# Kernel tuning notes

Measured on AMD Instinct MI355X. Metric: run time of the kernel, lower is better.

Reference implementation:

```python
import jax, jax.numpy as jnp
import numpy as np

B, N, T, NUM_API = 4, 160, 512, 20000  # queries, list length, tag vocab size, number of APIs
TAG_DENSITY = 0.05


def _compute_lambda(y_score, tag_set, M):
    # y_score: [N]; tag_set: [N,T] multi-hot rows api_tag_embedding[y_pred]; M: [T] multi-hot target.
    # Faithful to mode == 'cover' branch of LambdaRankLoss.compute_lambda.
    n = tag_set.shape[0]
    f32 = tag_set.dtype
    idx = jnp.arange(n)
    log_values = jnp.log2(jnp.arange(2, n + 2, dtype=f32))             # [N]
    P = jax.lax.cummax(tag_set, axis=0)                                # set_union_list = cummax(tag_set) [N,T]
    Mc = (jnp.count_nonzero(M) + 1).astype(f32)                        # M_nonzero_count
    # count_nonzero(clamp(M - set_union_list[k], min=0)) == #(M_t > P[k,t])
    cU = jnp.sum(M[None, :] > P, axis=1).astype(f32)                   # [N]

    # pre[i] = rowwise-max of tag_set[:i-1]. Torch quirk: i==0 -> tag_set[:-1] (all but last row); i==1 -> empty.
    pre = jnp.where(idx[:, None] == 0, P[n - 2][None, :],
                    jnp.where(idx[:, None] == 1, jnp.zeros((), f32),
                              P[jnp.clip(idx - 2, 0, n - 1)]))         # [N,T] (0 is max-identity: entries >= 0)

    # R[a,b] = max(tag_set[a..b]) along rows; 0 when b < a (rows before a masked to 0, then cummax)
    masked = jnp.where(idx[None, :, None] >= idx[:, None, None], tag_set[None, :, :], jnp.zeros((), f32))
    R = jax.lax.cummax(masked, axis=1)                                 # [N,N,T]

    # mid[k,i] = max(tag_set[i+1:k]) = R[i+1, k-1] when k >= i+2, else empty -> 0
    i_ix = idx[None, :]
    k_ix = idx[:, None]
    mid = jnp.where((k_ix >= i_ix + 2)[:, :, None],
                    R[jnp.clip(i_ix + 1, 0, n - 1), jnp.clip(k_ix - 1, 0, n - 1)],
                    jnp.zeros((), f32))                                # [K,I,T]

    # A[k,i] = max(cat(tag_set[:i-1], tag_set[i+1:k]));  Q[k,i,j] = max(A[k,i], tag_set[j])
    A = jnp.maximum(pre[None, :, :], mid)                              # [K,I,T]
    # count_nonzero(clamp(M - Q[k,i,j], 0)) = sum_t [M_t > A[k,i,t]] * [M_t > tag_set[j,t]]
    aM = (M[None, None, :] > A).astype(f32)                            # [K,I,T]
    bM = (M[None, :] > tag_set).astype(f32)                            # [J,T]
    cQ = jnp.einsum('kit,jt->kij', aM, bM)                             # [K,I,J] Q_nonzero counts

    W = (cU[:, None, None] - cQ) / (Mc * log_values[:, None, None])    # [K,I,J]
    # Z1[i,j] = sum_{k=i}^{j-1} W[k,i,j]  (strictly upper-triangular in (i,j))
    maskZ = (idx[None, :, None] <= idx[:, None, None]) & (idx[:, None, None] < idx[None, None, :])
    Z1 = jnp.sum(jnp.where(maskZ, W, jnp.zeros((), f32)), axis=0)      # [I,J]

    # lambda1[i,j] = 1 / (1 + exp(s_i - s_j))
    lam = 1.0 / (1.0 + jnp.exp(y_score[:, None] - y_score[None, :]))
    return jnp.sum(lam * Z1) / jnp.asarray(n + 1, f32)


def setup_inputs() -> dict:
    key = jax.random.key(0)
    k1, k2, k3, k4 = jax.random.split(key, 4)
    y_scores = jax.random.normal(k1, (B, N), jnp.float32)
    y_preds = jax.random.randint(k2, (B, N), 0, NUM_API)
    M = (jax.random.uniform(k3, (B, T)) < TAG_DENSITY).astype(jnp.float32)
    api_tag_embedding = (jax.random.uniform(k4, (NUM_API, T)) < TAG_DENSITY).astype(jnp.float32)
    return {"y_scores": y_scores, "M": M, "api_tag_embedding": api_tag_embedding, "y_preds": y_preds}


def reference(y_scores, M, api_tag_embedding, y_preds):
    def per_query(s, m, pred):
        return _compute_lambda(s, api_tag_embedding[pred], m)
    vals = jax.vmap(per_query)(y_scores, M, y_preds)  # [B]
    return jnp.mean(vals)  # loss / len(y_scores)
```

## Files before the change

### kernel.cpp

```cpp
#include <hip/hip_runtime.h>
#include <stdint.h>

typedef unsigned long long u64;

constexpr int B_ = 4;
constexpr int N_ = 160;
constexpr int T_ = 512;
constexpr int W_ = T_ / 64;

__global__ __launch_bounds__(64) void pack_tags(const float* __restrict__ emb,
                                                const int* __restrict__ preds,
                                                u64* __restrict__ tags,
                                                int* __restrict__ counter) {
    int row  = blockIdx.x;
    int lane = threadIdx.x;
    if (row == 0 && lane == 0) *counter = 0;
    const float* src = emb + (long long)preds[row] * T_;
#pragma unroll
    for (int w = 0; w < W_; ++w) {
        float v = src[w * 64 + lane];
        u64 m = __ballot(v != 0.0f);
        if (lane == 0) tags[(long long)row * W_ + w] = m;
    }
}

__global__ __launch_bounds__(256) void pack_scan(const float* __restrict__ Mf,
                                                 const u64* __restrict__ tags,
                                                 u64* __restrict__ Mp,
                                                 u64* __restrict__ P,
                                                 float* __restrict__ cU,
                                                 float* __restrict__ Mc) {
    __shared__ u64 S0[N_ * W_];
    __shared__ u64 S1[N_ * W_];
    __shared__ u64 Msh[W_];

    const int b    = blockIdx.x;
    const int tid  = threadIdx.x;
    const int lane = tid & 63;
    const int wv   = tid >> 6;

    for (int w = wv; w < W_; w += 4) {
        float v = Mf[(long long)b * T_ + w * 64 + lane];
        u64 m = __ballot(v != 0.0f);
        if (lane == 0) { Msh[w] = m; Mp[b * W_ + w] = m; }
    }
    for (int x = tid; x < N_ * W_; x += 256)
        S0[x] = tags[(long long)b * N_ * W_ + x];
    __syncthreads();

    u64* src = S0;
    u64* dst = S1;
    for (int d = 1; d < N_; d <<= 1) {
        for (int x = tid; x < N_ * W_; x += 256) {
            int r = x >> 3;
            u64 v = src[x];
            if (r >= d) v |= src[x - d * W_];
            dst[x] = v;
        }
        __syncthreads();
        u64* t = src; src = dst; dst = t;
    }

    for (int x = tid; x < N_ * W_; x += 256)
        P[(long long)b * N_ * W_ + x] = src[x];

    if (tid < N_) {
        int c = 0;
#pragma unroll
        for (int w = 0; w < W_; ++w)
            c += __popcll(Msh[w] & ~src[tid * W_ + w]);
        cU[b * N_ + tid] = (float)c;
    }
    if (tid == 0) {
        int c = 0;
#pragma unroll
        for (int w = 0; w < W_; ++w) c += __popcll(Msh[w]);
        Mc[b] = (float)(c + 1);
    }
}

__global__ __launch_bounds__(192) void lambda_main(const u64* __restrict__ tags,
                                                   const u64* __restrict__ Mp,
                                                   const u64* __restrict__ P,
                                                   const float* __restrict__ cU,
                                                   const float* __restrict__ Mc,
                                                   const float* __restrict__ scores,
                                                   double* __restrict__ partials,
                                                   int* __restrict__ counter,
                                                   float* __restrict__ out) {
    __shared__ u64 tagsL[N_ * W_];
    __shared__ u64 S0[N_ * W_];
    __shared__ u64 S1[N_ * W_];
    __shared__ u64 Msh[W_];
    __shared__ float scoresL[N_];
    __shared__ float redF[3];
    __shared__ int isLast;
    __shared__ double redD[3];

    const int k   = blockIdx.x;
    const int b   = blockIdx.y;
    const int tid = threadIdx.x;

    if (tid < W_) Msh[tid] = Mp[b * W_ + tid];
    for (int x = tid; x < N_; x += 192) scoresL[x] = scores[b * N_ + x];
    for (int x = tid; x < N_ * W_; x += 192)
        tagsL[x] = tags[(long long)b * N_ * W_ + x];
    __syncthreads();

    const int ne = k * W_;
    u64* src = S0;
    u64* dst = S1;
    for (int x = tid; x < ne; x += 192) src[x] = tagsL[x];
    __syncthreads();
    for (int d = 1; d < k; d <<= 1) {
        for (int x = tid; x < ne; x += 192) {
            int r = x >> 3;
            u64 v = src[x];
            if (r + d < k) v |= src[x + d * W_];
            dst[x] = v;
        }
        __syncthreads();
        u64* t = src; src = dst; dst = t;
    }

    u64* awL = dst;
    for (int x = tid; x < (k + 1) * W_; x += 192) {
        int i = x >> 3, w = x & 7;
        u64 pre;
        if (i == 1) pre = 0ull;
        else {
            int sr = (i == 0) ? (N_ - 2) : (i - 2);
            pre = P[((long long)b * N_ + sr) * W_ + w];
        }
        u64 sv = (i + 1 < k) ? src[(i + 1) * W_ + w] : 0ull;
        awL[x] = Msh[w] & ~pre & ~sv;
    }
    __syncthreads();

    const int m = N_ - 1 - k;
    float val = 0.0f;
    if (tid < m) {
        const int j = k + 1 + tid;
        u64 Bw[W_];
#pragma unroll
        for (int w = 0; w < W_; ++w) Bw[w] = Msh[w] & ~tagsL[j * W_ + w];
        const float sj  = scoresL[j];
        const float cUk = cU[b * N_ + k];
        float accLam = 0.0f, accC = 0.0f;
#pragma unroll 4
        for (int i = 0; i <= k; ++i) {
            int cc = 0;
#pragma unroll
            for (int w = 0; w < W_; ++w)
                cc += __popcll(awL[i * W_ + w] & Bw[w]);
            float lam = 1.0f / (1.0f + __expf(scoresL[i] - sj));
            accLam += lam;
            accC   += lam * (float)cc;
        }
        val = cUk * accLam - accC;
    }
    for (int off = 32; off >= 1; off >>= 1) val += __shfl_down(val, off, 64);
    if ((tid & 63) == 0) redF[tid >> 6] = val;
    __syncthreads();
    if (tid == 0) {
        float s = redF[0] + redF[1] + redF[2];
        float invlog = 1.0f / log2f((float)(k + 2));
        partials[b * N_ + k] = (double)(s * invlog) / (double)Mc[b];
        __threadfence();
        int done = atomicAdd(counter, 1);
        isLast = (done == N_ * B_ - 1) ? 1 : 0;
    }
    __syncthreads();

    if (isLast) {
        __threadfence();
        double s = 0.0;
        for (int x = tid; x < B_ * N_; x += 192) s += partials[x];
        for (int off = 32; off >= 1; off >>= 1) s += __shfl_down(s, off, 64);
        if ((tid & 63) == 0) redD[tid >> 6] = s;
        __syncthreads();
        if (tid == 0) {
            double t = redD[0] + redD[1] + redD[2];
            out[0] = (float)(t / ((double)(N_ + 1) * (double)B_));
        }
    }
}

extern "C" void kernel_launch(void* const* d_in, const int* in_sizes, int n_in,
                              void* d_out, int out_size, void* d_ws, size_t ws_size,
                              hipStream_t stream) {
    const float* y_scores = (const float*)d_in[0];
    const float* Mf       = (const float*)d_in[1];
    const float* emb      = (const float*)d_in[2];
    const int*   preds    = (const int*)d_in[3];
    float* out = (float*)d_out;

    u64* tags = (u64*)d_ws;
    u64* P    = tags + (size_t)B_ * N_ * W_;
    u64* Mp   = P + (size_t)B_ * N_ * W_;
    double* partials = (double*)(Mp + B_ * W_);
    float* cU = (float*)(partials + B_ * N_);
    float* Mc = cU + B_ * N_;
    int* counter = (int*)(Mc + B_);

    pack_tags<<<B_ * N_, 64, 0, stream>>>(emb, preds, tags, counter);
    pack_scan<<<B_, 256, 0, stream>>>(Mf, tags, Mp, P, cU, Mc);
    dim3 grid(N_, B_);
    lambda_main<<<grid, 192, 0, stream>>>(tags, Mp, P, cU, Mc, y_scores,
                                          partials, counter, out);
}
```

Before: 131.7 us.

## Batch four k values per block with register-tiled popcount and incremental AW updates

Each block of the main kernel now handles four consecutive k values instead of one. It rebuilds the prefix-OR scan in shared memory using a transposed, padded layout, which removes the separate per-batch scan kernel and its global round trip. For each later k it updates the AND-NOT masks incrementally instead of rescanning, and computes the i×j pair sums with 2x2 register tiles to reuse loaded words. The costs are far fewer blocks (less parallelism across CUs), a serial loop over k with block barriers, and the full prefix scan repeated in every block.

```diff
diff --git a/kernel.cpp b/kernel.cpp
--- a/kernel.cpp
+++ b/kernel.cpp
@@ -7,6 +7,9 @@
 constexpr int N_ = 160;
 constexpr int T_ = 512;
 constexpr int W_ = T_ / 64;
+constexpr int LDP_ = N_ + 1;
+constexpr int KC_ = 4;
+constexpr int NBLK_ = N_ / KC_;
 
 __global__ __launch_bounds__(64) void pack_tags(const float* __restrict__ emb,
                                                 const int* __restrict__ preds,
@@ -24,163 +27,181 @@
     }
 }
 
-__global__ __launch_bounds__(256) void pack_scan(const float* __restrict__ Mf,
-                                                 const u64* __restrict__ tags,
-                                                 u64* __restrict__ Mp,
-                                                 u64* __restrict__ P,
-                                                 float* __restrict__ cU,
-                                                 float* __restrict__ Mc) {
-    __shared__ u64 S0[N_ * W_];
-    __shared__ u64 S1[N_ * W_];
-    __shared__ u64 Msh[W_];
-
-    const int b    = blockIdx.x;
-    const int tid  = threadIdx.x;
-    const int lane = tid & 63;
-    const int wv   = tid >> 6;
-
-    for (int w = wv; w < W_; w += 4) {
-        float v = Mf[(long long)b * T_ + w * 64 + lane];
-        u64 m = __ballot(v != 0.0f);
-        if (lane == 0) { Msh[w] = m; Mp[b * W_ + w] = m; }
-    }
-    for (int x = tid; x < N_ * W_; x += 256)
-        S0[x] = tags[(long long)b * N_ * W_ + x];
-    __syncthreads();
-
-    u64* src = S0;
-    u64* dst = S1;
-    for (int d = 1; d < N_; d <<= 1) {
-        for (int x = tid; x < N_ * W_; x += 256) {
-            int r = x >> 3;
-            u64 v = src[x];
-            if (r >= d) v |= src[x - d * W_];
-            dst[x] = v;
-        }
-        __syncthreads();
-        u64* t = src; src = dst; dst = t;
-    }
-
-    for (int x = tid; x < N_ * W_; x += 256)
-        P[(long long)b * N_ * W_ + x] = src[x];
-
-    if (tid < N_) {
-        int c = 0;
-#pragma unroll
-        for (int w = 0; w < W_; ++w)
-            c += __popcll(Msh[w] & ~src[tid * W_ + w]);
-        cU[b * N_ + tid] = (float)c;
-    }
-    if (tid == 0) {
-        int c = 0;
-#pragma unroll
-        for (int w = 0; w < W_; ++w) c += __popcll(Msh[w]);
-        Mc[b] = (float)(c + 1);
-    }
-}
-
-__global__ __launch_bounds__(192) void lambda_main(const u64* __restrict__ tags,
+__global__ __launch_bounds__(256) void lambda_main(const u64* __restrict__ tags,
                                                    const u64* __restrict__ Mp,
-                                                   const u64* __restrict__ P,
-                                                   const float* __restrict__ cU,
-                                                   const float* __restrict__ Mc,
                                                    const float* __restrict__ scores,
                                                    double* __restrict__ partials,
                                                    int* __restrict__ counter,
                                                    float* __restrict__ out) {
-    __shared__ u64 tagsL[N_ * W_];
-    __shared__ u64 S0[N_ * W_];
-    __shared__ u64 S1[N_ * W_];
+    __shared__ u64 T[W_ * LDP_];
+    __shared__ u64 BT[W_ * LDP_];
+    __shared__ u64 PA[W_ * LDP_];
+    __shared__ u64 PB[W_ * LDP_];
+    __shared__ u64 PC[W_ * LDP_];
     __shared__ u64 Msh[W_];
     __shared__ float scoresL[N_];
-    __shared__ float redF[3];
+    __shared__ float redF[KC_][4];
+    __shared__ double redD[4];
     __shared__ int isLast;
-    __shared__ double redD[3];
-
-    const int k   = blockIdx.x;
+
+    const int kc  = blockIdx.x;
     const int b   = blockIdx.y;
     const int tid = threadIdx.x;
-
-    if (tid < W_) Msh[tid] = Mp[b * W_ + tid];
-    for (int x = tid; x < N_; x += 192) scoresL[x] = scores[b * N_ + x];
-    for (int x = tid; x < N_ * W_; x += 192)
-        tagsL[x] = tags[(long long)b * N_ * W_ + x];
-    __syncthreads();
-
-    const int ne = k * W_;
-    u64* src = S0;
-    u64* dst = S1;
-    for (int x = tid; x < ne; x += 192) src[x] = tagsL[x];
-    __syncthreads();
-    for (int d = 1; d < k; d <<= 1) {
-        for (int x = tid; x < ne; x += 192) {
+    const int k0  = kc * KC_;
+    const int myw = tid & 7;
+    const int lane = tid & 63;
+    const int wv   = tid >> 6;
+
+    const u64 Mw = Mp[b * W_ + myw];
+    if (tid < W_) Msh[tid] = Mw;
+    for (int x = tid; x < N_; x += 256) scoresL[x] = scores[b * N_ + x];
+
+    const u64* tg = tags + (long long)b * N_ * W_;
+    for (int x = tid; x < N_ * W_; x += 256) {
+        int r = x >> 3;
+        u64 v = tg[x];
+        T[myw * LDP_ + r]  = v;
+        PA[myw * LDP_ + r] = v;
+        if (r > k0) BT[myw * LDP_ + r] = Mw & ~v;
+    }
+    __syncthreads();
+
+    u64* PP;
+    {
+        u64 *s = PA, *d = PB;
+        for (int dd = 1; dd < N_; dd <<= 1) {
+            for (int x = tid; x < N_ * W_; x += 256) {
+                int r = x >> 3;
+                u64 v = s[myw * LDP_ + r];
+                if (r >= dd) v |= s[myw * LDP_ + r - dd];
+                d[myw * LDP_ + r] = v;
+            }
+            __syncthreads();
+            u64* t = s; s = d; d = t;
+        }
+        PP = s;
+    }
+    u64* freeP = (PP == PA) ? PB : PA;
+
+    u64 *S = freeP, *D = PC;
+    for (int x = tid; x < k0 * W_; x += 256)
+        S[myw * LDP_ + (x >> 3)] = T[myw * LDP_ + (x >> 3)];
+    __syncthreads();
+    for (int dd = 1; dd < k0; dd <<= 1) {
+        for (int x = tid; x < k0 * W_; x += 256) {
             int r = x >> 3;
-            u64 v = src[x];
-            if (r + d < k) v |= src[x + d * W_];
-            dst[x] = v;
+            u64 v = S[myw * LDP_ + r];
+            if (r + dd < k0) v |= S[myw * LDP_ + r + dd];
+            D[myw * LDP_ + r] = v;
         }
         __syncthreads();
-        u64* t = src; src = dst; dst = t;
-    }
-
-    u64* awL = dst;
-    for (int x = tid; x < (k + 1) * W_; x += 192) {
-        int i = x >> 3, w = x & 7;
-        u64 pre;
-        if (i == 1) pre = 0ull;
-        else {
-            int sr = (i == 0) ? (N_ - 2) : (i - 2);
-            pre = P[((long long)b * N_ + sr) * W_ + w];
-        }
-        u64 sv = (i + 1 < k) ? src[(i + 1) * W_ + w] : 0ull;
-        awL[x] = Msh[w] & ~pre & ~sv;
-    }
-    __syncthreads();
-
-    const int m = N_ - 1 - k;
-    float val = 0.0f;
-    if (tid < m) {
-        const int j = k + 1 + tid;
-        u64 Bw[W_];
-#pragma unroll
-        for (int w = 0; w < W_; ++w) Bw[w] = Msh[w] & ~tagsL[j * W_ + w];
-        const float sj  = scoresL[j];
-        const float cUk = cU[b * N_ + k];
-        float accLam = 0.0f, accC = 0.0f;
-#pragma unroll 4
-        for (int i = 0; i <= k; ++i) {
-            int cc = 0;
+        u64* t = S; S = D; D = t;
+    }
+    u64* AWp = D;
+
+    for (int x = tid; x < (k0 + 1) * W_; x += 256) {
+        int i = x >> 3;
+        u64 pre = (i == 1) ? 0ull
+                : PP[myw * LDP_ + ((i == 0) ? (N_ - 2) : (i - 2))];
+        u64 sv  = (i + 1 < k0) ? S[myw * LDP_ + i + 1] : 0ull;
+        AWp[myw * LDP_ + i] = Mw & ~pre & ~sv;
+    }
+    __syncthreads();
+
+    float val[KC_] = {0.f, 0.f, 0.f, 0.f};
+    for (int kk = 0; kk < KC_; ++kk) {
+        const int k = k0 + kk;
+        const int m = N_ - 1 - k;
+        if (m > 0) {
+            int cci = 0;
 #pragma unroll
             for (int w = 0; w < W_; ++w)
-                cc += __popcll(awL[i * W_ + w] & Bw[w]);
-            float lam = 1.0f / (1.0f + __expf(scoresL[i] - sj));
-            accLam += lam;
-            accC   += lam * (float)cc;
-        }
-        val = cUk * accLam - accC;
-    }
-    for (int off = 32; off >= 1; off >>= 1) val += __shfl_down(val, off, 64);
-    if ((tid & 63) == 0) redF[tid >> 6] = val;
+                cci += __popcll(Msh[w] & ~PP[w * LDP_ + k]);
+            const float cUk = (float)cci;
+
+            const int nTj = (m + 1) >> 1;
+            const int nTi = (k + 2) >> 1;
+            const int ntiles = nTi * nTj;
+            const int dTi = 256 / nTj;
+            const int rTj = 256 - dTi * nTj;
+            int ti = tid / nTj;
+            int tj = tid - ti * nTj;
+            float aL = 0.f, aC = 0.f;
+            for (int t = tid; t < ntiles; t += 256) {
+                const int i0 = ti << 1;
+                const int j0 = k + 1 + (tj << 1);
+                const bool vi = (i0 + 1 <= k);
+                const bool vj = (j0 + 1 < N_);
+                const int i1 = vi ? i0 + 1 : i0;
+                const int j1 = vj ? j0 + 1 : j0;
+                int c00 = 0, c01 = 0, c10 = 0, c11 = 0;
+#pragma unroll
+                for (int w = 0; w < W_; ++w) {
+                    u64 a0 = AWp[w * LDP_ + i0], a1 = AWp[w * LDP_ + i1];
+                    u64 b0 = BT[w * LDP_ + j0],  b1 = BT[w * LDP_ + j1];
+                    c00 += __popcll(a0 & b0); c01 += __popcll(a0 & b1);
+                    c10 += __popcll(a1 & b0); c11 += __popcll(a1 & b1);
+                }
+                const float si0 = scoresL[i0], si1 = scoresL[i1];
+                const float sj0 = scoresL[j0], sj1 = scoresL[j1];
+                float l00 = 1.f / (1.f + __expf(si0 - sj0));
+                float l01 = 1.f / (1.f + __expf(si0 - sj1)); if (!vj) l01 = 0.f;
+                float l10 = 1.f / (1.f + __expf(si1 - sj0)); if (!vi) l10 = 0.f;
+                float l11 = 1.f / (1.f + __expf(si1 - sj1)); if (!(vi && vj)) l11 = 0.f;
+                aL += l00 + l01 + l10 + l11;
+                aC += l00 * (float)c00 + l01 * (float)c01
+                    + l10 * (float)c10 + l11 * (float)c11;
+                ti += dTi; tj += rTj;
+                if (tj >= nTj) { tj -= nTj; ++ti; }
+            }
+            val[kk] = cUk * aL - aC;
+        }
+        if (kk < KC_ - 1) {
+            __syncthreads();
+            const u64 tk = T[myw * LDP_ + k];
+            for (int x = tid; x < k * W_; x += 256)
+                AWp[myw * LDP_ + (x >> 3)] &= ~tk;
+            if (tid < W_) {
+                const int i = k + 1;
+                u64 pre = (i == 1) ? 0ull : PP[tid * LDP_ + i - 2];
+                AWp[tid * LDP_ + i] = Msh[tid] & ~pre;
+            }
+            __syncthreads();
+        }
+    }
+
+#pragma unroll
+    for (int kk = 0; kk < KC_; ++kk) {
+        float v = val[kk];
+        for (int off = 32; off >= 1; off >>= 1) v += __shfl_down(v, off, 64);
+        if (lane == 0) redF[kk][wv] = v;
+    }
+    __syncthreads();
+    if (tid < KC_) {
+        const int k = k0 + tid;
+        float s = redF[tid][0] + redF[tid][1] + redF[tid][2] + redF[tid][3];
+        int mc = 1;
+#pragma unroll
+        for (int w = 0; w < W_; ++w) mc += __popcll(Msh[w]);
+        partials[b * N_ + k] = (double)(s / log2f((float)(k + 2))) / (double)mc;
+    }
     __syncthreads();
     if (tid == 0) {
-        float s = redF[0] + redF[1] + redF[2];
-        float invlog = 1.0f / log2f((float)(k + 2));
-        partials[b * N_ + k] = (double)(s * invlog) / (double)Mc[b];
         __threadfence();
         int done = atomicAdd(counter, 1);
-        isLast = (done == N_ * B_ - 1) ? 1 : 0;
+        isLast = (done == NBLK_ * B_ - 1) ? 1 : 0;
     }
     __syncthreads();
 
     if (isLast) {
         __threadfence();
         double s = 0.0;
-        for (int x = tid; x < B_ * N_; x += 192) s += partials[x];
+        for (int x = tid; x < B_ * N_; x += 256) s += partials[x];
         for (int off = 32; off >= 1; off >>= 1) s += __shfl_down(s, off, 64);
-        if ((tid & 63) == 0) redD[tid >> 6] = s;
+        if (lane == 0) redD[wv] = s;
         __syncthreads();
         if (tid == 0) {
-            double t = redD[0] + redD[1] + redD[2];
+            double t = redD[0] + redD[1] + redD[2] + redD[3];
             out[0] = (float)(t / ((double)(N_ + 1) * (double)B_));
         }
     }
@@ -196,16 +217,26 @@
     float* out = (float*)d_out;
 
     u64* tags = (u64*)d_ws;
-    u64* P    = tags + (size_t)B_ * N_ * W_;
-    u64* Mp   = P + (size_t)B_ * N_ * W_;
-    double* partials = (double*)(Mp + B_ * W_);
-    float* cU = (float*)(partials + B_ * N_);
-    float* Mc = cU + B_ * N_;
-    int* counter = (int*)(Mc + B_);
+    u64* Mp   = tags + (size_t)B_ * N_ * W_;
+    double* partials = (double*)(Mp + (size_t)B_ * W_);
+    int* counter = (int*)(partials + B_ * N_);
+
+    struct Launcher {
+        static __global__ __launch_bounds__(64) void packM(const float* Mf,
+                                                           u64* Mp) {
+            int b = blockIdx.x, lane = threadIdx.x;
+#pragma unroll
+            for (int w = 0; w < W_; ++w) {
+                float v = Mf[(long long)b * T_ + w * 64 + lane];
+                u64 m = __ballot(v != 0.0f);
+                if (lane == 0) Mp[b * W_ + w] = m;
+            }
+        }
+    };
 
     pack_tags<<<B_ * N_, 64, 0, stream>>>(emb, preds, tags, counter);
-    pack_scan<<<B_, 256, 0, stream>>>(Mf, tags, Mp, P, cU, Mc);
-    dim3 grid(N_, B_);
-    lambda_main<<<grid, 192, 0, stream>>>(tags, Mp, P, cU, Mc, y_scores,
+    Launcher::packM<<<B_, 64, 0, stream>>>(Mf, Mp);
+    dim3 grid(NBLK_, B_);
+    lambda_main<<<grid, 256, 0, stream>>>(tags, Mp, y_scores,
                                           partials, counter, out);
 }
```

Result: faster. 122.7 us (-6.9%).

## Tile lambda inner loop 2x2 over (i,j) with transposed shared bitmasks

Applied to the files above, without the earlier changes.

The main kernel's per-block work is now spread over all (i,j) pairs in 2x2 register tiles across 256 threads, replacing the old scheme of one thread per j looping over i. That scheme left many threads idle for large k. The aw and B bitmasks are stored transposed in padded shared arrays so each tile reuses its loads across four popcounts. Packing of M moves into the tag-packing kernel, and the M mask is kept in registers. The cost is more index arithmetic, edge masking for odd tile sizes, and higher shared memory use per block.

```diff
diff --git a/kernel.cpp b/kernel.cpp
--- a/kernel.cpp
+++ b/kernel.cpp
@@ -7,43 +7,49 @@
 constexpr int N_ = 160;
 constexpr int T_ = 512;
 constexpr int W_ = T_ / 64;
-
-__global__ __launch_bounds__(64) void pack_tags(const float* __restrict__ emb,
-                                                const int* __restrict__ preds,
-                                                u64* __restrict__ tags,
-                                                int* __restrict__ counter) {
-    int row  = blockIdx.x;
-    int lane = threadIdx.x;
+constexpr int LDP_ = N_ + 1;
+
+__global__ __launch_bounds__(64) void pack_all(const float* __restrict__ emb,
+                                               const int* __restrict__ preds,
+                                               const float* __restrict__ Mf,
+                                               u64* __restrict__ tags,
+                                               u64* __restrict__ Mp,
+                                               int* __restrict__ counter) {
+    const int row  = blockIdx.x;
+    const int lane = threadIdx.x;
     if (row == 0 && lane == 0) *counter = 0;
-    const float* src = emb + (long long)preds[row] * T_;
-#pragma unroll
-    for (int w = 0; w < W_; ++w) {
-        float v = src[w * 64 + lane];
-        u64 m = __ballot(v != 0.0f);
-        if (lane == 0) tags[(long long)row * W_ + w] = m;
-    }
-}
-
-__global__ __launch_bounds__(256) void pack_scan(const float* __restrict__ Mf,
-                                                 const u64* __restrict__ tags,
-                                                 u64* __restrict__ Mp,
+    if (row < B_ * N_) {
+        const float* src = emb + (long long)preds[row] * T_;
+#pragma unroll
+        for (int w = 0; w < W_; ++w) {
+            u64 m = __ballot(src[w * 64 + lane] != 0.0f);
+            if (lane == 0) tags[(long long)row * W_ + w] = m;
+        }
+    } else {
+        const int b = row - B_ * N_;
+#pragma unroll
+        for (int w = 0; w < W_; ++w) {
+            u64 m = __ballot(Mf[(long long)b * T_ + w * 64 + lane] != 0.0f);
+            if (lane == 0) Mp[b * W_ + w] = m;
+        }
+    }
+}
+
+__global__ __launch_bounds__(256) void pack_scan(const u64* __restrict__ tags,
+                                                 const u64* __restrict__ Mp,
                                                  u64* __restrict__ P,
                                                  float* __restrict__ cU,
                                                  float* __restrict__ Mc) {
     __shared__ u64 S0[N_ * W_];
     __shared__ u64 S1[N_ * W_];
-    __shared__ u64 Msh[W_];
-
-    const int b    = blockIdx.x;
-    const int tid  = threadIdx.x;
-    const int lane = tid & 63;
-    const int wv   = tid >> 6;
-
-    for (int w = wv; w < W_; w += 4) {
-        float v = Mf[(long long)b * T_ + w * 64 + lane];
-        u64 m = __ballot(v != 0.0f);
-        if (lane == 0) { Msh[w] = m; Mp[b * W_ + w] = m; }
-    }
+
+    const int b   = blockIdx.x;
+    const int tid = threadIdx.x;
+
+    u64 Mr[W_];
+#pragma unroll
+    for (int w = 0; w < W_; ++w) Mr[w] = Mp[b * W_ + w];
+
     for (int x = tid; x < N_ * W_; x += 256)
         S0[x] = tags[(long long)b * N_ * W_ + x];
     __syncthreads();
@@ -68,18 +74,18 @@
         int c = 0;
 #pragma unroll
         for (int w = 0; w < W_; ++w)
-            c += __popcll(Msh[w] & ~src[tid * W_ + w]);
+            c += __popcll(Mr[w] & ~src[tid * W_ + w]);
         cU[b * N_ + tid] = (float)c;
     }
     if (tid == 0) {
         int c = 0;
 #pragma unroll
-        for (int w = 0; w < W_; ++w) c += __popcll(Msh[w]);
+        for (int w = 0; w < W_; ++w) c += __popcll(Mr[w]);
         Mc[b] = (float)(c + 1);
     }
 }
 
-__global__ __launch_bounds__(192) void lambda_main(const u64* __restrict__ tags,
+__global__ __launch_bounds__(256) void lambda_main(const u64* __restrict__ tags,
                                                    const u64* __restrict__ Mp,
                                                    const u64* __restrict__ P,
                                                    const float* __restrict__ cU,
@@ -88,32 +94,38 @@
                                                    double* __restrict__ partials,
                                                    int* __restrict__ counter,
                                                    float* __restrict__ out) {
-    __shared__ u64 tagsL[N_ * W_];
     __shared__ u64 S0[N_ * W_];
     __shared__ u64 S1[N_ * W_];
-    __shared__ u64 Msh[W_];
+    __shared__ u64 awT[W_ * LDP_];
+    __shared__ u64 bT[W_ * LDP_];
     __shared__ float scoresL[N_];
-    __shared__ float redF[3];
+    __shared__ float redF[4];
+    __shared__ double redD[4];
     __shared__ int isLast;
-    __shared__ double redD[3];
 
     const int k   = blockIdx.x;
     const int b   = blockIdx.y;
     const int tid = threadIdx.x;
-
-    if (tid < W_) Msh[tid] = Mp[b * W_ + tid];
-    for (int x = tid; x < N_; x += 192) scoresL[x] = scores[b * N_ + x];
-    for (int x = tid; x < N_ * W_; x += 192)
-        tagsL[x] = tags[(long long)b * N_ * W_ + x];
-    __syncthreads();
-
-    const int ne = k * W_;
+    const int m   = N_ - 1 - k;
+
+    u64 Mr[W_];
+#pragma unroll
+    for (int w = 0; w < W_; ++w) Mr[w] = Mp[b * W_ + w];
+
+    for (int x = tid; x < N_; x += 256) scoresL[x] = scores[b * N_ + x];
+
+    const u64* tg = tags + (long long)b * N_ * W_;
+    for (int x = tid; x < k * W_; x += 256) S0[x] = tg[x];
+    for (int x = tid; x < m * W_; x += 256) {
+        int j = k + 1 + (x >> 3), w = x & 7;
+        bT[w * LDP_ + j] = Mr[w] & ~tg[j * W_ + w];
+    }
+    __syncthreads();
+
     u64* src = S0;
     u64* dst = S1;
-    for (int x = tid; x < ne; x += 192) src[x] = tagsL[x];
-    __syncthreads();
     for (int d = 1; d < k; d <<= 1) {
-        for (int x = tid; x < ne; x += 192) {
+        for (int x = tid; x < k * W_; x += 256) {
             int r = x >> 3;
             u64 v = src[x];
             if (r + d < k) v |= src[x + d * W_];
@@ -123,8 +135,7 @@
         u64* t = src; src = dst; dst = t;
     }
 
-    u64* awL = dst;
-    for (int x = tid; x < (k + 1) * W_; x += 192) {
+    for (int x = tid; x < (k + 1) * W_; x += 256) {
         int i = x >> 3, w = x & 7;
         u64 pre;
         if (i == 1) pre = 0ull;
@@ -133,37 +144,56 @@
             pre = P[((long long)b * N_ + sr) * W_ + w];
         }
         u64 sv = (i + 1 < k) ? src[(i + 1) * W_ + w] : 0ull;
-        awL[x] = Msh[w] & ~pre & ~sv;
-    }
-    __syncthreads();
-
-    const int m = N_ - 1 - k;
+        awT[w * LDP_ + i] = Mr[w] & ~pre & ~sv;
+    }
+    __syncthreads();
+
     float val = 0.0f;
-    if (tid < m) {
-        const int j = k + 1 + tid;
-        u64 Bw[W_];
-#pragma unroll
-        for (int w = 0; w < W_; ++w) Bw[w] = Msh[w] & ~tagsL[j * W_ + w];
-        const float sj  = scoresL[j];
+    if (m > 0) {
         const float cUk = cU[b * N_ + k];
-        float accLam = 0.0f, accC = 0.0f;
-#pragma unroll 4
-        for (int i = 0; i <= k; ++i) {
-            int cc = 0;
-#pragma unroll
-            for (int w = 0; w < W_; ++w)
-                cc += __popcll(awL[i * W_ + w] & Bw[w]);
-            float lam = 1.0f / (1.0f + __expf(scoresL[i] - sj));
-            accLam += lam;
-            accC   += lam * (float)cc;
-        }
-        val = cUk * accLam - accC;
-    }
+        const int nTj = (m + 1) >> 1;
+        const int nTi = (k + 2) >> 1;
+        const int ntiles = nTi * nTj;
+        const int dTi = 256 / nTj;
+        const int rTj = 256 - dTi * nTj;
+        int ti = tid / nTj;
+        int tj = tid - ti * nTj;
+        float aL = 0.f, aC = 0.f;
+        for (int t = tid; t < ntiles; t += 256) {
+            const int i0 = ti << 1;
+            const int j0 = k + 1 + (tj << 1);
+            const bool vi = (i0 + 1 <= k);
+            const bool vj = (j0 + 1 < N_);
+            const int i1 = vi ? i0 + 1 : i0;
+            const int j1 = vj ? j0 + 1 : j0;
+            int c00 = 0, c01 = 0, c10 = 0, c11 = 0;
+#pragma unroll
+            for (int w = 0; w < W_; ++w) {
+                u64 a0 = awT[w * LDP_ + i0], a1 = awT[w * LDP_ + i1];
+                u64 b0 = bT[w * LDP_ + j0],  b1 = bT[w * LDP_ + j1];
+                c00 += __popcll(a0 & b0); c01 += __popcll(a0 & b1);
+                c10 += __popcll(a1 & b0); c11 += __popcll(a1 & b1);
+            }
+            const float si0 = scoresL[i0], si1 = scoresL[i1];
+            const float sj0 = scoresL[j0], sj1 = scoresL[j1];
+            float l00 = 1.f / (1.f + __expf(si0 - sj0));
+            float l01 = 1.f / (1.f + __expf(si0 - sj1)); if (!vj) l01 = 0.f;
+            float l10 = 1.f / (1.f + __expf(si1 - sj0)); if (!vi) l10 = 0.f;
+            float l11 = 1.f / (1.f + __expf(si1 - sj1)); if (!(vi && vj)) l11 = 0.f;
+            aL += l00 + l01 + l10 + l11;
+            aC += l00 * (float)c00 + l01 * (float)c01
+                + l10 * (float)c10 + l11 * (float)c11;
+            ti += dTi; tj += rTj;
+            if (tj >= nTj) { tj -= nTj; ++ti; }
+        }
+        val = cUk * aL - aC;
+    }
+
     for (int off = 32; off >= 1; off >>= 1) val += __shfl_down(val, off, 64);
     if ((tid & 63) == 0) redF[tid >> 6] = val;
     __syncthreads();
     if (tid == 0) {
-        float s = redF[0] + redF[1] + redF[2];
+        float s = redF[0] + redF[1] + redF[2] + redF[3];
         float invlog = 1.0f / log2f((float)(k + 2));
         partials[b * N_ + k] = (double)(s * invlog) / (double)Mc[b];
         __threadfence();
@@ -175,12 +205,12 @@
     if (isLast) {
         __threadfence();
         double s = 0.0;
-        for (int x = tid; x < B_ * N_; x += 192) s += partials[x];
+        for (int x = tid; x < B_ * N_; x += 256) s += partials[x];
         for (int off = 32; off >= 1; off >>= 1) s += __shfl_down(s, off, 64);
         if ((tid & 63) == 0) redD[tid >> 6] = s;
         __syncthreads();
         if (tid == 0) {
-            double t = redD[0] + redD[1] + redD[2];
+            double t = redD[0] + redD[1] + redD[2] + redD[3];
             out[0] = (float)(t / ((double)(N_ + 1) * (double)B_));
         }
     }
@@ -203,9 +233,9 @@
     float* Mc = cU + B_ * N_;
     int* counter = (int*)(Mc + B_);
 
-    pack_tags<<<B_ * N_, 64, 0, stream>>>(emb, preds, tags, counter);
-    pack_scan<<<B_, 256, 0, stream>>>(Mf, tags, Mp, P, cU, Mc);
+    pack_all<<<B_ * N_ + B_, 64, 0, stream>>>(emb, preds, Mf, tags, Mp, counter);
+    pack_scan<<<B_, 256, 0, stream>>>(tags, Mp, P, cU, Mc);
     dim3 grid(N_, B_);
-    lambda_main<<<grid, 192, 0, stream>>>(tags, Mp, P, cU, Mc, y_scores,
+    lambda_main<<<grid, 256, 0, stream>>>(tags, Mp, P, cU, Mc, y_scores,
                                           partials, counter, out);
 }
```

After: 119.7 us. 9.2% less time.
